# Performance work log

Measured on AMD Instinct MI355X. Metric: run time of the kernel, lower is better.

Reference implementation:

```python
import jax, jax.numpy as jnp
from jax import lax
import numpy as np

NUM_SCALES = 4
NUM_ORI = 8
SIGMA = 2.0
FILTER_SIZE = 32  # min(512 // 2**scale, 32) == 32 for all scales, already even
J = 4
POOL = 2 ** J  # 16


def _make_gabor_filters():
    """Replicates GaborWavelet2D + _init_wavelet_filters. Returns (real, imag) stacks
    of shape [num_scales*num_ori, 1, FILTER_SIZE, FILTER_SIZE]."""
    oris = np.linspace(0.0, np.pi, NUM_ORI)
    idx = np.arange(FILTER_SIZE, dtype=np.float32) - FILTER_SIZE // 2
    X, Y = np.meshgrid(idx, idx, indexing='ij')
    reals, imags = [], []
    for scale in range(1, NUM_SCALES + 1):
        for o in oris:
            Xr = X * np.cos(o) + Y * np.sin(o)
            Yr = -X * np.sin(o) + Y * np.cos(o)
            sf = scale * SIGMA
            env = np.exp(-0.5 * (Xr ** 2 + Yr ** 2) / sf ** 2)
            phase = 2.0 * np.pi * (1.0 / scale) * Xr / sf
            reals.append(env * np.cos(phase))
            imags.append(env * np.sin(phase))
    real = np.stack(reals).astype(np.float32)[:, None]  # [32,1,32,32]
    imag = np.stack(imags).astype(np.float32)[:, None]
    return real, imag


def setup_inputs() -> dict:
    key = jax.random.key(0)
    x = jax.random.normal(key, (8, 3, 512, 512), dtype=jnp.float32)
    w_real, w_imag = _make_gabor_filters()
    return {"x": x, "w_real": jnp.asarray(w_real), "w_imag": jnp.asarray(w_imag)}


def _avg_pool(t):
    # torch F.avg_pool2d(kernel=16), default stride=kernel, floor mode (drop remainder)
    B, C, H, W = t.shape
    Ho, Wo = H // POOL, W // POOL
    t = t[:, :, :Ho * POOL, :Wo * POOL]
    return t.reshape(B, C, Ho, POOL, Wo, POOL).mean(axis=(3, 5))


def reference(x, w_real, w_imag):
    # x: [B,3,512,512]
    x_gray = x.mean(axis=1, keepdims=True)  # [B,1,H,W]
    S0 = _avg_pool(x_gray)  # [B,1,32,32]

    pad = FILTER_SIZE // 2  # 16 -> conv output is (H+1, W+1) = 513x513
    w = jnp.concatenate([w_real, w_imag], axis=0)  # [64,1,32,32]
    conv = lax.conv_general_dilated(
        x_gray, w, window_strides=(1, 1), padding=((pad, pad), (pad, pad)),
        dimension_numbers=('NCHW', 'OIHW', 'NCHW'))  # [B,64,513,513], cross-correlation like torch
    nf = w_real.shape[0]
    cr, ci = conv[:, :nf], conv[:, nf:]
    mag = jnp.sqrt(cr ** 2 + ci ** 2 + 1e-8)  # [B,32,513,513]
    S1 = _avg_pool(mag)  # [B,32,32,32]
    return (S0, S1)
```

## Files before the change

kernel.cpp:

```cpp
#include <hip/hip_runtime.h>
#include <math.h>

#define IMG   512
#define NFILT 32
#define NPAIR 16
#define PI_F  3.14159265358979323846f
#define GS    104

typedef _Float16 v8h __attribute__((ext_vector_type(8)));
typedef float    v4f __attribute__((ext_vector_type(4)));

__device__ __forceinline__ unsigned pkrtz(float a, float b) {
    typedef __fp16 f16x2 __attribute__((ext_vector_type(2)));
    union { f16x2 h; unsigned u; } x;
    x.h = __builtin_amdgcn_cvt_pkrtz(a, b);
    return x.u;
}

template <int CTRL>
__device__ __forceinline__ float dpp_add(float v) {
    int t = __builtin_amdgcn_update_dpp(0, __float_as_int(v), CTRL, 0xf, 0xf, true);
    return v + __int_as_float(t);
}

#if __has_builtin(__builtin_amdgcn_sqrtf)
__device__ __forceinline__ float fsqrt(float x) { return __builtin_amdgcn_sqrtf(x); }
#else
__device__ __forceinline__ float fsqrt(float x) { return sqrtf(x); }
#endif

__device__ __forceinline__ void bar_lgkm() {
    asm volatile("s_waitcnt lgkmcnt(0)\n\ts_barrier" ::: "memory");
}

__device__ __forceinline__ v8h ldfrag(const uint4* p) {
    union { uint4 u; v8h h; } x; x.u = *p; return x.h;
}

__global__ void make_tables(unsigned* __restrict__ tabs) {
    __shared__ _Float16 P[5][168];
    const int fo = blockIdx.x;
    const int tid = threadIdx.x;
    for (int e = tid; e < 5 * 168; e += 256) ((_Float16*)P)[e] = (_Float16)0.0f;
    __syncthreads();
    if (tid < 160) {
        int tbl = tid >> 5, t = tid & 31;
        int s = (fo >> 3) + 1, o = fo & 7;
        float theta = (float)o * (PI_F / 7.0f);
        float sf = (float)s * 2.0f;
        float kf = 2.0f * PI_F / ((float)s * sf);
        float a = kf * cosf(theta), b = kf * sinf(theta);
        float d = (float)(t - 16);
        float env = expf(-0.5f * d * d / (sf * sf));
        float v;
        switch (tbl) {
            case 0: v =  env * cosf(b * d); break;
            case 1: v =  env * sinf(b * d); break;
            case 2: v =  env * cosf(a * d); break;
            case 3: v =  env * sinf(a * d); break;
            default: v = -env * sinf(a * d); break;
        }
        P[tbl][t + 64] = (_Float16)v;
    }
    __syncthreads();
    unsigned* dst = tabs + (size_t)fo * 3200;
    for (int e = tid; e < 3200; e += 256) {
        int tbl  = e / 640;  int rem2 = e - tbl * 640;
        int copy = rem2 / 80; int idw = rem2 - copy * 80;
        int p0 = (idw >> 2) * 8 + copy + (idw & 3) * 2;
        union { unsigned u; _Float16 h[2]; } p;
        p.h[0] = P[tbl][p0];
        p.h[1] = P[tbl][p0 + 1];
        dst[e] = p.u;
    }
}

__launch_bounds__(512, 4)
__global__ void conv_kernel(const float* __restrict__ x,
                            const uint4* __restrict__ tabs,
                            float* __restrict__ s0out,
                            float* __restrict__ s1out) {
    __shared__ _Float16 gray[96 * GS];
    __shared__ _Float16 Tre[2][64 * GS];
    __shared__ _Float16 Tim[2][64 * GS];
    __shared__ float    s1st[NFILT * 16];

    const int bx = blockIdx.x;
    const int n  = bx >> 6;
    const int t6 = bx & 63;
    const int ty = t6 >> 3, tx = t6 & 7;
    const int r0g = ty * 64 - 16;
    const int c0g = tx * 64 - 16;
    const int tid = threadIdx.x;

    const int lane = tid & 63;
    const int w    = tid >> 6;
    const int r4   = w & 3;
    const int half = w >> 2;
    const int nn   = lane & 15;
    const int q8   = (lane >> 4) << 3;
    const int q4   = (lane >> 4) << 2;
    const int cr   = r4 * 16 + nn;
    const int u    = q8 - cr + 64;
    const int b0   = r4 >> 1;
    const int uoff = (u & 7) * 20 + (u >> 3);
    const int hx8  = (((lane >> 4) ^ (nn & 3)) << 3);
    const int crx3 = cr & 3;

    const uint4* fb0 = tabs + uoff;
    v8h Gre0[2], Gim0[2], Fre[2], Fim[2];
    #pragma unroll
    for (int j = 0; j < 2; ++j) {
        int idx = (b0 + j) * 4;
        Gre0[j] = ldfrag(fb0 + idx);
        Gim0[j] = ldfrag(fb0 + 160 + idx);
        Fre[j]  = ldfrag(fb0 + 320 + idx);
        Fim[j]  = ldfrag(fb0 + 480 + idx);
    }

    {
        const float* c0p = x + (size_t)n * 3 * IMG * IMG;
        const float* c1p = c0p + IMG * IMG;
        const float* c2p = c0p + 2 * IMG * IMG;
        for (int e = tid; e < 96 * 24; e += 512) {
            int hr = e / 24, g4 = e - hr * 24;
            int hc0 = g4 * 4;
            int gr = r0g + hr, gc0 = c0g + hc0;
            float4 v = make_float4(0.f, 0.f, 0.f, 0.f);
            if (hr < 95 && (unsigned)gr < IMG && (unsigned)gc0 < IMG) {
                size_t off = ((size_t)gr * IMG + gc0) >> 2;
                float4 a = ((const float4*)c0p)[off];
                float4 b = ((const float4*)c1p)[off];
                float4 c = ((const float4*)c2p)[off];
                v.x = (a.x + b.x + c.x) * (1.0f / 3.0f);
                v.y = (a.y + b.y + c.y) * (1.0f / 3.0f);
                v.z = (a.z + b.z + c.z) * (1.0f / 3.0f);
                v.w = (hc0 == 92) ? 0.0f : (a.w + b.w + c.w) * (1.0f / 3.0f);
            }
            uint2 w2;
            w2.x = pkrtz(v.x, v.y);
            w2.y = pkrtz(v.z, v.w);
            *(uint2*)(&gray[hr * GS + hc0]) = w2;
        }
    }
    __syncthreads();

    if (tid < 256) {
        int cell = tid >> 4, sub = tid & 15;
        int pr = cell >> 2, pc = cell & 3;
        const _Float16* row = &gray[(16 + pr * 16 + sub) * GS + 16 + pc * 16];
        float s = 0.0f;
        #pragma unroll
        for (int j = 0; j < 16; ++j) s += (float)row[j];
        s += __shfl_xor(s, 1);
        s += __shfl_xor(s, 2);
        s += __shfl_xor(s, 4);
        s += __shfl_xor(s, 8);
        if (sub == 0)
            s0out[(size_t)n * 1024 + (ty * 4 + pr) * 32 + (tx * 4 + pc)] = s * (1.0f / 256.0f);
    }

    v8h Agray[3][2];
    #pragma unroll
    for (int mi = 0; mi < 3; ++mi)
        #pragma unroll
        for (int j = 0; j < 2; ++j)
            Agray[mi][j] = *(const v8h*)(&gray[((half * 3 + mi) * 16 + nn) * GS + (b0 + j) * 32 + q8]);

    #pragma unroll
    for (int mi = 0; mi < 3; ++mi) {
        int mt = half * 3 + mi;
        v4f aR = {0.f, 0.f, 0.f, 0.f}, aI = {0.f, 0.f, 0.f, 0.f};
        #pragma unroll
        for (int j = 0; j < 2; ++j) {
            aR = __builtin_amdgcn_mfma_f32_16x16x32_f16(Agray[mi][j], Gre0[j], aR, 0, 0, 0);
            aI = __builtin_amdgcn_mfma_f32_16x16x32_f16(Agray[mi][j], Gim0[j], aI, 0, 0, 0);
        }
        int gw = (((mt << 1) | (q4 >> 3)) ^ crx3);
        int wo = cr * GS + gw * 8 + (q4 & 7);
        uint2 pr, pi;
        pr.x = pkrtz(aR[0], aR[1]);  pr.y = pkrtz(aR[2], aR[3]);
        pi.x = pkrtz(aI[0], aI[1]);  pi.y = pkrtz(aI[2], aI[3]);
        *(uint2*)(&Tre[0][wo]) = pr;
        *(uint2*)(&Tim[0][wo]) = pi;
    }
    __syncthreads();

    for (int p = 0; p < NPAIR; ++p) {
        const _Float16* Tr  = Tre[p & 1];
        const _Float16* Ti  = Tim[p & 1];
        _Float16*       Trn = Tre[(p + 1) & 1];
        _Float16*       Tin = Tim[(p + 1) & 1];
        const int fa  = ((p >> 2) << 3) + (p & 3);
        const int fbi = ((p >> 2) << 3) + 7 - (p & 3);
        const int nxp = (p < NPAIR - 1) ? p + 1 : p;
        const int nxfa = ((nxp >> 2) << 3) + (nxp & 3);
        const uint4* fbn = tabs + (size_t)nxfa * 800 + uoff;

        v8h Gre[2], Gim[2];
        #pragma unroll
        for (int j = 0; j < 2; ++j) {
            int idx = (b0 + j) * 4;
            Gre[j] = ldfrag(fbn + idx);
            Gim[j] = ldfrag(fbn + 160 + idx);
        }

        #pragma unroll
        for (int ni = 0; ni < 2; ++ni) {
            int nt = half * 2 + ni;
            v4f P1 = {0.f, 0.f, 0.f, 0.f}, P2 = {0.f, 0.f, 0.f, 0.f};
            v4f P3 = {0.f, 0.f, 0.f, 0.f}, P4 = {0.f, 0.f, 0.f, 0.f};
            #pragma unroll
            for (int j = 0; j < 2; ++j) {
                int ro = (nt * 16 + nn) * GS + (b0 + j) * 32 + hx8;
                v8h tR = *(const v8h*)(&Tr[ro]);
                v8h tI = *(const v8h*)(&Ti[ro]);
                P1 = __builtin_amdgcn_mfma_f32_16x16x32_f16(Fre[j], tR, P1, 0, 0, 0);
                P2 = __builtin_amdgcn_mfma_f32_16x16x32_f16(Fim[j], tI, P2, 0, 0, 0);
                P3 = __builtin_amdgcn_mfma_f32_16x16x32_f16(Fre[j], tI, P3, 0, 0, 0);
                P4 = __builtin_amdgcn_mfma_f32_16x16x32_f16(Fim[j], tR, P4, 0, 0, 0);
            }
            const v4f eps4 = {1e-8f, 1e-8f, 1e-8f, 1e-8f};
            v4f s4 = P1 * P1 + eps4;
            s4 = P2 * P2 + s4;
            s4 = P3 * P3 + s4;
            s4 = P4 * P4 + s4;
            v4f t4 = P1 * P2 - P3 * P4;
            t4 = t4 + t4;
            v4f na = s4 - t4, nb = s4 + t4;
            float sa0 = fsqrt(fmaxf(na[0], 1e-8f));
            float sa1 = fsqrt(fmaxf(na[1], 1e-8f));
            float sa2 = fsqrt(fmaxf(na[2], 1e-8f));
            float sa3 = fsqrt(fmaxf(na[3], 1e-8f));
            float sb0 = fsqrt(fmaxf(nb[0], 1e-8f));
            float sb1 = fsqrt(fmaxf(nb[1], 1e-8f));
            float sb2 = fsqrt(fmaxf(nb[2], 1e-8f));
            float sb3 = fsqrt(fmaxf(nb[3], 1e-8f));
            float ma = (sa0 + sa1) + (sa2 + sa3);
            float mb = (sb0 + sb1) + (sb2 + sb3);
            ma = dpp_add<0xB1>(ma);   mb = dpp_add<0xB1>(mb);
            ma = dpp_add<0x4E>(ma);   mb = dpp_add<0x4E>(mb);
            ma = dpp_add<0x141>(ma);  mb = dpp_add<0x141>(mb);
            ma = dpp_add<0x140>(ma);  mb = dpp_add<0x140>(mb);
            ma += __shfl_xor(ma, 16); mb += __shfl_xor(mb, 16);
            ma += __shfl_xor(ma, 32); mb += __shfl_xor(mb, 32);
            if (lane == 0) {
                s1st[fa  * 16 + r4 * 4 + nt] = ma;
                s1st[fbi * 16 + r4 * 4 + nt] = mb;
            }
        }

        if (p < NPAIR - 1) {
            #pragma unroll
            for (int mi = 0; mi < 3; ++mi) {
                int mt = half * 3 + mi;
                v4f aR = {0.f, 0.f, 0.f, 0.f}, aI = {0.f, 0.f, 0.f, 0.f};
                #pragma unroll
                for (int j = 0; j < 2; ++j) {
                    aR = __builtin_amdgcn_mfma_f32_16x16x32_f16(Agray[mi][j], Gre[j], aR, 0, 0, 0);
                    aI = __builtin_amdgcn_mfma_f32_16x16x32_f16(Agray[mi][j], Gim[j], aI, 0, 0, 0);
                }
                int gw = (((mt << 1) | (q4 >> 3)) ^ crx3);
                int wo = cr * GS + gw * 8 + (q4 & 7);
                uint2 pr, pi;
                pr.x = pkrtz(aR[0], aR[1]);  pr.y = pkrtz(aR[2], aR[3]);
                pi.x = pkrtz(aI[0], aI[1]);  pi.y = pkrtz(aI[2], aI[3]);
                *(uint2*)(&Trn[wo]) = pr;
                *(uint2*)(&Tin[wo]) = pi;
            }
            #pragma unroll
            for (int j = 0; j < 2; ++j) {
                int idx = (b0 + j) * 4;
                Fre[j] = ldfrag(fbn + 320 + idx);
                Fim[j] = ldfrag(fbn + 480 + idx);
            }
        }
        bar_lgkm();
    }

    float* s1b = s1out + (size_t)n * NFILT * 32 * 32;
    for (int e = tid; e < NFILT * 16; e += 512) {
        int fi = e >> 4, cell = e & 15;
        int r4c = cell >> 2, ntc = cell & 3;
        s1b[((size_t)fi * 32 + (ty * 4 + r4c)) * 32 + (tx * 4 + ntc)] =
            s1st[e] * (1.0f / 256.0f);
    }
}

extern "C" void kernel_launch(void* const* d_in, const int* in_sizes, int n_in,
                              void* d_out, int out_size, void* d_ws, size_t ws_size,
                              hipStream_t stream) {
    const float* x = (const float*)d_in[0];
    float* out = (float*)d_out;
    unsigned* tabs = (unsigned*)d_ws;

    hipLaunchKernelGGL(make_tables, dim3(32), dim3(256), 0, stream, tabs);
    hipLaunchKernelGGL(conv_kernel, dim3(512), dim3(512), 0, stream,
                       x, (const uint4*)tabs, out, out + 8192);
}
```

Baseline: 118.3 us.

## Drop LDS XOR swizzle and replace cross-group shuffles with LDS partial sums

Removes the XOR swizzle on the T-tile LDS layout, so writes and reads now use plain row-major offsets. Replaces the two cross-lane __shfl_xor reductions with a per-16-lane-group store into a 4x larger LDS staging buffer, and sums the four partials in the final output loop. The aim is fewer cross-lane ops and less address arithmetic in the hot loop. The unswizzled layout with a 104-element row stride may bring back LDS bank conflicts that the swizzle had avoided.

```diff
diff --git a/kernel.cpp b/kernel.cpp
--- a/kernel.cpp
+++ b/kernel.cpp
@@ -83,7 +83,7 @@
     __shared__ _Float16 gray[96 * GS];
     __shared__ _Float16 Tre[2][64 * GS];
     __shared__ _Float16 Tim[2][64 * GS];
-    __shared__ float    s1st[NFILT * 16];
+    __shared__ float    s1st4[NFILT * 16 * 4];
 
     const int bx = blockIdx.x;
     const int n  = bx >> 6;
@@ -104,8 +104,7 @@
     const int u    = q8 - cr + 64;
     const int b0   = r4 >> 1;
     const int uoff = (u & 7) * 20 + (u >> 3);
-    const int hx8  = (((lane >> 4) ^ (nn & 3)) << 3);
-    const int crx3 = cr & 3;
+    const int grp  = lane >> 4;
 
     const uint4* fb0 = tabs + uoff;
     v8h Gre0[2], Gim0[2], Fre[2], Fim[2];
@@ -176,13 +175,12 @@
             aR = __builtin_amdgcn_mfma_f32_16x16x32_f16(Agray[mi][j], Gre0[j], aR, 0, 0, 0);
             aI = __builtin_amdgcn_mfma_f32_16x16x32_f16(Agray[mi][j], Gim0[j], aI, 0, 0, 0);
         }
-        int gw = (((mt << 1) | (q4 >> 3)) ^ crx3);
-        int wo = cr * GS + gw * 8 + (q4 & 7);
+        int mb = mt * 16 + q4;
         uint2 pr, pi;
         pr.x = pkrtz(aR[0], aR[1]);  pr.y = pkrtz(aR[2], aR[3]);
         pi.x = pkrtz(aI[0], aI[1]);  pi.y = pkrtz(aI[2], aI[3]);
-        *(uint2*)(&Tre[0][wo]) = pr;
-        *(uint2*)(&Tim[0][wo]) = pi;
+        *(uint2*)(&Tre[0][cr * GS + mb]) = pr;
+        *(uint2*)(&Tim[0][cr * GS + mb]) = pi;
     }
     __syncthreads();
 
@@ -212,7 +210,7 @@
             v4f P3 = {0.f, 0.f, 0.f, 0.f}, P4 = {0.f, 0.f, 0.f, 0.f};
             #pragma unroll
             for (int j = 0; j < 2; ++j) {
-                int ro = (nt * 16 + nn) * GS + (b0 + j) * 32 + hx8;
+                int ro = (nt * 16 + nn) * GS + (b0 + j) * 32 + q8;
                 v8h tR = *(const v8h*)(&Tr[ro]);
                 v8h tI = *(const v8h*)(&Ti[ro]);
                 P1 = __builtin_amdgcn_mfma_f32_16x16x32_f16(Fre[j], tR, P1, 0, 0, 0);
@@ -242,11 +240,9 @@
             ma = dpp_add<0x4E>(ma);   mb = dpp_add<0x4E>(mb);
             ma = dpp_add<0x141>(ma);  mb = dpp_add<0x141>(mb);
             ma = dpp_add<0x140>(ma);  mb = dpp_add<0x140>(mb);
-            ma += __shfl_xor(ma, 16); mb += __shfl_xor(mb, 16);
-            ma += __shfl_xor(ma, 32); mb += __shfl_xor(mb, 32);
-            if (lane == 0) {
-                s1st[fa  * 16 + r4 * 4 + nt] = ma;
-                s1st[fbi * 16 + r4 * 4 + nt] = mb;
+            if ((lane & 15) == 0) {
+                s1st4[(fa  * 16 + r4 * 4 + nt) * 4 + grp] = ma;
+                s1st4[(fbi * 16 + r4 * 4 + nt) * 4 + grp] = mb;
             }
         }
 
@@ -260,13 +256,12 @@
                     aR = __builtin_amdgcn_mfma_f32_16x16x32_f16(Agray[mi][j], Gre[j], aR, 0, 0, 0);
                     aI = __builtin_amdgcn_mfma_f32_16x16x32_f16(Agray[mi][j], Gim[j], aI, 0, 0, 0);
                 }
-                int gw = (((mt << 1) | (q4 >> 3)) ^ crx3);
-                int wo = cr * GS + gw * 8 + (q4 & 7);
+                int mb = mt * 16 + q4;
                 uint2 pr, pi;
                 pr.x = pkrtz(aR[0], aR[1]);  pr.y = pkrtz(aR[2], aR[3]);
                 pi.x = pkrtz(aI[0], aI[1]);  pi.y = pkrtz(aI[2], aI[3]);
-                *(uint2*)(&Trn[wo]) = pr;
-                *(uint2*)(&Tin[wo]) = pi;
+                *(uint2*)(&Trn[cr * GS + mb]) = pr;
+                *(uint2*)(&Tin[cr * GS + mb]) = pi;
             }
             #pragma unroll
             for (int j = 0; j < 2; ++j) {
@@ -282,8 +277,10 @@
     for (int e = tid; e < NFILT * 16; e += 512) {
         int fi = e >> 4, cell = e & 15;
         int r4c = cell >> 2, ntc = cell & 3;
+        v4f pp = *(const v4f*)(&s1st4[e * 4]);
+        float s = (pp[0] + pp[1]) + (pp[2] + pp[3]);
         s1b[((size_t)fi * 32 + (ty * 4 + r4c)) * 32 + (tx * 4 + ntc)] =
-            s1st[e] * (1.0f / 256.0f);
+            s * (1.0f / 256.0f);
     }
 }
 
```

Measured after the change: 114.1 us. 1.04x faster.
